# Performance work log

Measured on AMD Instinct MI355X. Metric: run time of the kernel, lower is better.

The kernel has to match this reference:

```python
import jax, jax.numpy as jnp
import numpy as np

EMBED = 1024

def setup_inputs() -> dict:
    key = jax.random.key(0)
    kx, kq, kk, kv = jax.random.split(key, 4)
    x = jax.random.normal(kx, (4, 2048, EMBED), dtype=jnp.float32)
    s = 1.0 / np.sqrt(EMBED)
    Wq = jax.random.normal(kq, (EMBED, EMBED), dtype=jnp.float32) * s
    Wk = jax.random.normal(kk, (EMBED, EMBED), dtype=jnp.float32) * s
    Wv = jax.random.normal(kv, (EMBED, EMBED), dtype=jnp.float32) * s
    return {"x": x, "Wq": Wq, "Wk": Wk, "Wv": Wv}

def reference(x, Wq, Wk, Wv):
    # x: [b, s, e]; nn.Linear(y) = y @ W.T, weights stored [out, in]
    Q = jnp.einsum('bse,oe->bso', x, Wq)
    K = jnp.einsum('bse,oe->bso', x, Wk)
    V = jnp.einsum('bse,oe->bso', x, Wv)
    scale = 1.0 / jnp.sqrt(jnp.asarray(x.shape[-1], x.dtype))
    energy = jnp.einsum('bqe,bke->bqk', Q, K) * scale  # [b, s, s]
    attention = jax.nn.softmax(energy, axis=-1)
    out = jnp.einsum('bqk,bke->bqe', attention, V)
    return out
```

## Files before the change

### kernel.cpp

```cpp
#include <hip/hip_runtime.h>
#include <stdint.h>


typedef __attribute__((ext_vector_type(8))) short bf16x8;
typedef __attribute__((ext_vector_type(4))) float f32x4;

__device__ __forceinline__ float bf2f(uint16_t u) {
    return __uint_as_float(((uint32_t)u) << 16);
}
__device__ __forceinline__ uint16_t f2bf(float f) {
    uint32_t u = __float_as_uint(f);
    uint32_t r = u + 0x7FFFu + ((u >> 16) & 1u);
    return (uint16_t)(r >> 16);
}

__device__ __forceinline__ void gll16(const void* g, void* l) {
    __builtin_amdgcn_global_load_lds(
        (const __attribute__((address_space(1))) uint32_t*)g,
        (__attribute__((address_space(3))) uint32_t*)l,
        16, 0, 0);
}

__global__ __launch_bounds__(256) void cast_all(const float* __restrict__ x,
                                                const float* __restrict__ Wq,
                                                const float* __restrict__ Wk,
                                                const float* __restrict__ Wv,
                                                uint16_t* __restrict__ xb,
                                                uint16_t* __restrict__ wqkvb,
                                                int NX4, int NW4) {
    int i = blockIdx.x * 256 + threadIdx.x;
    const float* src;
    uint16_t* dst;
    int off;
    if (i < NX4) {
        src = x; dst = xb; off = i;
    } else {
        int j = i - NX4;
        if (j >= 3 * NW4) return;
        int which = j / NW4;
        off = j - which * NW4;
        src = (which == 0) ? Wq : (which == 1) ? Wk : Wv;
        dst = wqkvb + (size_t)which * NW4 * 4;
    }
    float4 v = ((const float4*)src)[off];
    ushort4 o;
    o.x = f2bf(v.x); o.y = f2bf(v.y); o.z = f2bf(v.z); o.w = f2bf(v.w);
    ((ushort4*)dst)[off] = o;
}

__global__ __launch_bounds__(256) void softmax_rows(uint16_t* __restrict__ P) {
    const int n = 2048;
    uint16_t* row = P + (size_t)blockIdx.x * n;
    int tid = threadIdx.x;
    int w = tid >> 6, ln = tid & 63;
    float v[8];
    float m = -3.4e38f;
    #pragma unroll
    for (int i = 0; i < 8; i++) { v[i] = bf2f(row[tid + 256 * i]); m = fmaxf(m, v[i]); }
    #pragma unroll
    for (int o = 32; o >= 1; o >>= 1) m = fmaxf(m, __shfl_down(m, o, 64));
    __shared__ float smax[4], ssum[4];
    if (ln == 0) smax[w] = m;
    __syncthreads();
    m = fmaxf(fmaxf(smax[0], smax[1]), fmaxf(smax[2], smax[3]));
    float s = 0.f;
    #pragma unroll
    for (int i = 0; i < 8; i++) { v[i] = __expf(v[i] - m); s += v[i]; }
    #pragma unroll
    for (int o = 32; o >= 1; o >>= 1) s += __shfl_down(s, o, 64);
    if (ln == 0) ssum[w] = s;
    __syncthreads();
    s = ssum[0] + ssum[1] + ssum[2] + ssum[3];
    float inv = 1.f / s;
    #pragma unroll
    for (int i = 0; i < 8; i++) row[tid + 256 * i] = f2bf(v[i] * inv);
}

#define BM 128
#define BN 128
#define BK 32

template <typename OutT>
__global__ __launch_bounds__(256) void gemm_nt(const uint16_t* __restrict__ A,
                                               const uint16_t* __restrict__ B,
                                               OutT* __restrict__ C,
                                               int gx, int gy,
                                               long lda, long ldb, long ldc,
                                               int K, float alpha,
                                               long sA, long sB, long sC,
                                               uint16_t* __restrict__ VtP,
                                               int vcol0) {
    const int total = gridDim.x;
    const int n     = blockIdx.x;
    const int per   = total >> 3;
    const int g     = (n & 7) * per + (n >> 3);
    const int pb    = gx * gy;
    const int bz    = g / pb;
    const int r     = g - bz * pb;
    const int stpr  = gx >> 3;
    const int st    = r >> 6;
    const int w     = r & 63;
    const int sty   = st / stpr;
    const int stx   = st - sty * stpr;
    const int bx    = (stx << 3) + (w & 7);
    const int by    = (sty << 3) + (w >> 3);

    A += (long)bz * sA;
    B += (long)bz * sB;
    C += (long)bz * sC;

    __shared__ uint16_t As[3][BM * BK];
    __shared__ uint16_t Bs[3][BM * BK];

    const int tid  = threadIdx.x;
    const int m0   = by * BM;
    const int n0   = bx * BN;
    const int wave = tid >> 6;
    const int lane = tid & 63;
    const int quad = lane >> 4;
    const int l16  = lane & 15;
    const int wr   = (wave >> 1) * 64;
    const int wc   = (wave & 1) * 64;

    const int sr = tid >> 2;
    const int sc = (tid & 3) * 8;
    const uint16_t* Ag = A + (long)(m0 + sr) * lda + sc;
    const uint16_t* Bg = B + (long)(n0 + sr) * ldb + sc;
    const long rsA = 64 * lda;
    const long rsB = 64 * ldb;
    const int so0 = sr * BK + sc;
    const int so1 = (sr + 64) * BK + sc;

    const int nk = K / BK;

    gll16(Ag,       &As[0][so0]);
    gll16(Ag + rsA, &As[0][so1]);
    gll16(Bg,       &Bs[0][so0]);
    gll16(Bg + rsB, &Bs[0][so1]);
    Ag += BK; Bg += BK;
    gll16(Ag,       &As[1][so0]);
    gll16(Ag + rsA, &As[1][so1]);
    gll16(Bg,       &Bs[1][so0]);
    gll16(Bg + rsB, &Bs[1][so1]);
    Ag += BK; Bg += BK;

    f32x4 acc[4][4] = {};
    int cur = 0, pf = 2;

    for (int k = 0; k < nk; ++k) {
        if (k < nk - 1) {
            asm volatile("s_waitcnt vmcnt(4)\n\ts_barrier" ::: "memory");
        } else {
            asm volatile("s_waitcnt vmcnt(0)\n\ts_barrier" ::: "memory");
        }

        if (k + 2 < nk) {
            gll16(Ag,       &As[pf][so0]);
            gll16(Ag + rsA, &As[pf][so1]);
            gll16(Bg,       &Bs[pf][so0]);
            gll16(Bg + rsB, &Bs[pf][so1]);
            Ag += BK; Bg += BK;
        }

        const uint16_t* Ac = As[cur];
        const uint16_t* Bc = Bs[cur];
        const int ko = quad * 8;
        bf16x8 af[4], bfr[4];
        #pragma unroll
        for (int i = 0; i < 4; i++)
            af[i] = *(const bf16x8*)(&Ac[(wr + i * 16 + l16) * BK + ko]);
        #pragma unroll
        for (int j = 0; j < 4; j++)
            bfr[j] = *(const bf16x8*)(&Bc[(wc + j * 16 + l16) * BK + ko]);
        #pragma unroll
        for (int i = 0; i < 4; i++)
            #pragma unroll
            for (int j = 0; j < 4; j++)
                acc[i][j] = __builtin_amdgcn_mfma_f32_16x16x32_bf16(af[i], bfr[j], acc[i][j], 0, 0, 0);

        cur = (cur == 2) ? 0 : cur + 1;
        pf  = (pf  == 2) ? 0 : pf + 1;
    }

    if (VtP && n0 >= vcol0) {
        #pragma unroll
        for (int i = 0; i < 4; i++) {
            const int row0 = m0 + wr + i * 16 + quad * 4;
            const int b    = row0 >> 11;
            const int s    = row0 & 2047;
            #pragma unroll
            for (int j = 0; j < 4; j++) {
                const int e = n0 + wc + j * 16 + l16 - vcol0;
                ushort4 o;
                o.x = f2bf(acc[i][j][0]);
                o.y = f2bf(acc[i][j][1]);
                o.z = f2bf(acc[i][j][2]);
                o.w = f2bf(acc[i][j][3]);
                *(ushort4*)(VtP + ((long)b * 1024 + e) * 2048 + s) = o;
            }
        }
    } else {
        #pragma unroll
        for (int i = 0; i < 4; i++) {
            #pragma unroll
            for (int j = 0; j < 4; j++) {
                #pragma unroll
                for (int r4 = 0; r4 < 4; r4++) {
                    int row = m0 + wr + i * 16 + quad * 4 + r4;
                    int col = n0 + wc + j * 16 + l16;
                    float val = acc[i][j][r4] * alpha;
                    if constexpr (sizeof(OutT) == 2)
                        C[(long)row * ldc + col] = f2bf(val);
                    else
                        C[(long)row * ldc + col] = val;
                }
            }
        }
    }
}

extern "C" void kernel_launch(void* const* d_in, const int* in_sizes, int n_in,
                              void* d_out, int out_size, void* d_ws, size_t ws_size,
                              hipStream_t stream) {
    const float* x  = (const float*)d_in[0];
    const float* Wq = (const float*)d_in[1];
    const float* Wk = (const float*)d_in[2];
    const float* Wv = (const float*)d_in[3];
    float* out = (float*)d_out;

    const int Bn = 4, S = 2048, E = 1024;
    const long MS = (long)Bn * S;
    const int  N3 = 3 * E;

    char* ws = (char*)d_ws;
    uint16_t* xb    = (uint16_t*)ws;  ws += (size_t)MS * E * 2;
    uint16_t* wqkvb = (uint16_t*)ws;  ws += (size_t)N3 * E * 2;
    uint16_t* QKb   = (uint16_t*)ws;  ws += (size_t)MS * 2048 * 2;
    uint16_t* Vt    = (uint16_t*)ws;  ws += (size_t)Bn * E * S * 2;
    uint16_t* Pb    = (uint16_t*)ws;  ws += (size_t)Bn * S * S * 2;

    dim3 blk(256);

    {
        int NX4 = (int)(MS * E / 4);
        int NW4 = E * E / 4;
        int tot = NX4 + 3 * NW4;
        cast_all<<<dim3((tot + 255) / 256), blk, 0, stream>>>(
            x, Wq, Wk, Wv, xb, wqkvb, NX4, NW4);
    }

    {
        int gx = N3 / BN, gy = (int)(MS / BM);
        gemm_nt<uint16_t><<<dim3(gx * gy), blk, 0, stream>>>(
            xb, wqkvb, QKb, gx, gy, E, E, 2048, E, 1.f, 0, 0, 0,
            Vt, 2048);
    }

    {
        int gx = S / BN, gy = S / BM;
        gemm_nt<uint16_t><<<dim3(gx * gy * Bn), blk, 0, stream>>>(
            QKb, QKb + 1024, Pb, gx, gy, 2048, 2048, S, E, 0.03125f,
            (long)S * 2048, (long)S * 2048, (long)S * S,
            nullptr, 0);
    }

    softmax_rows<<<dim3(Bn * S), blk, 0, stream>>>(Pb);

    {
        int gx = E / BN, gy = S / BM;
        gemm_nt<float><<<dim3(gx * gy * Bn), blk, 0, stream>>>(
            Pb, Vt, out, gx, gy, S, S, E, S, 1.f,
            (long)S * S, (long)E * S, (long)S * E,
            nullptr, 0);
    }
}
```

Before: 273.7 us.

## Rewrite GEMM with 256-wide tiles, 8 waves, swizzled LDS and phased MFMA scheduling

The bf16 NT GEMM moves from 128x128x32 tiles with 4 waves and a triple buffer to 256x256 (or 128x256) tiles with BK=64, 8 waves, and a double buffer. LDS rows are XOR-swizzled to avoid bank conflicts. Loads and MFMAs are interleaved in four phases, using s_setprio and barriers to overlap global prefetch with compute. The larger tiles cut global traffic per FLOP, but they raise register and LDS pressure and lower block count, so the grid may be too small to fill the CUs.

```diff
diff --git a/kernel.cpp b/kernel.cpp
--- a/kernel.cpp
+++ b/kernel.cpp
@@ -19,6 +19,14 @@
         (const __attribute__((address_space(1))) uint32_t*)g,
         (__attribute__((address_space(3))) uint32_t*)l,
         16, 0, 0);
+}
+
+template <int NC>
+__device__ __forceinline__ void stageT(const uint16_t* g, long stride,
+                                       uint16_t* l, int tid) {
+    #pragma unroll
+    for (int c = 0; c < NC; ++c)
+        gll16(g + (long)c * 64 * stride, l + c * 4096 + tid * 8);
 }
 
 __global__ __launch_bounds__(256) void cast_all(const float* __restrict__ x,
@@ -76,139 +84,152 @@
     for (int i = 0; i < 8; i++) row[tid + 256 * i] = f2bf(v[i] * inv);
 }
 
-#define BM 128
-#define BN 128
-#define BK 32
-
-template <typename OutT>
-__global__ __launch_bounds__(256) void gemm_nt(const uint16_t* __restrict__ A,
-                                               const uint16_t* __restrict__ B,
-                                               OutT* __restrict__ C,
-                                               int gx, int gy,
-                                               long lda, long ldb, long ldc,
-                                               int K, float alpha,
-                                               long sA, long sB, long sC,
-                                               uint16_t* __restrict__ VtP,
-                                               int vcol0) {
+
+#define DS_A(mh_) do { \
+    _Pragma("unroll") for (int f_ = 0; f_ < MH; ++f_) { \
+        const uint16_t* p_ = Asb + axbase + ((mh_)*MH + f_) * 1024; \
+        af[f_][0] = *(const bf16x8*)(p_ + cs0); \
+        af[f_][1] = *(const bf16x8*)(p_ + cs1); \
+    } } while (0)
+
+#define DS_B(nh_) do { \
+    _Pragma("unroll") for (int n_ = 0; n_ < 2; ++n_) { \
+        const uint16_t* p_ = Bsb + bxbase + ((nh_)*2 + n_) * 1024; \
+        bf[nh_][n_][0] = *(const bf16x8*)(p_ + cs0); \
+        bf[nh_][n_][1] = *(const bf16x8*)(p_ + cs1); \
+    } } while (0)
+
+#define MMA(mh_, nh_) do { \
+    _Pragma("unroll") for (int f_ = 0; f_ < MH; ++f_) { \
+        _Pragma("unroll") for (int n_ = 0; n_ < 2; ++n_) { \
+            acc[(mh_)*MH + f_][(nh_)*2 + n_] = __builtin_amdgcn_mfma_f32_16x16x32_bf16( \
+                af[f_][0], bf[nh_][n_][0], acc[(mh_)*MH + f_][(nh_)*2 + n_], 0, 0, 0); \
+            acc[(mh_)*MH + f_][(nh_)*2 + n_] = __builtin_amdgcn_mfma_f32_16x16x32_bf16( \
+                af[f_][1], bf[nh_][n_][1], acc[(mh_)*MH + f_][(nh_)*2 + n_], 0, 0, 0); \
+        } } } while (0)
+
+#define PH_ENTER do { \
+    asm volatile("s_barrier\n\ts_waitcnt lgkmcnt(0)" ::: "memory"); \
+    __builtin_amdgcn_s_setprio(1); } while (0)
+
+#define PH_EXIT do { \
+    __builtin_amdgcn_s_setprio(0); \
+    asm volatile("s_barrier" ::: "memory"); } while (0)
+
+template <int BM, typename OutT>
+__global__ __launch_bounds__(512, 2) void gemm_nt(const uint16_t* __restrict__ A,
+                                                  const uint16_t* __restrict__ B,
+                                                  OutT* __restrict__ C,
+                                                  int gx, int gy,
+                                                  long lda, long ldb, long ldc,
+                                                  int K, float alpha,
+                                                  long sA, long sB, long sC,
+                                                  uint16_t* __restrict__ VtP,
+                                                  int vcol0) {
+    constexpr int MF  = BM / 32;
+    constexpr int MH  = MF / 2;
+    constexpr int NAC = BM / 64;
+
     const int total = gridDim.x;
-    const int n     = blockIdx.x;
-    const int per   = total >> 3;
-    const int g     = (n & 7) * per + (n >> 3);
-    const int pb    = gx * gy;
-    const int bz    = g / pb;
-    const int r     = g - bz * pb;
-    const int stpr  = gx >> 3;
-    const int st    = r >> 6;
-    const int w     = r & 63;
-    const int sty   = st / stpr;
-    const int stx   = st - sty * stpr;
-    const int bx    = (stx << 3) + (w & 7);
-    const int by    = (sty << 3) + (w >> 3);
+    const int nb  = blockIdx.x;
+    const int per = total >> 3;
+    const int g   = (nb & 7) * per + (nb >> 3);
+    const int pb  = gx * gy;
+    const int bz  = g / pb;
+    const int r   = g - bz * pb;
+    const int stpr = gx >> 2;
+    const int st  = r >> 4;
+    const int w   = r & 15;
+    const int sty = st / stpr;
+    const int stx = st - sty * stpr;
+    const int bx  = (stx << 2) + (w & 3);
+    const int by  = (sty << 2) + (w >> 2);
 
     A += (long)bz * sA;
     B += (long)bz * sB;
     C += (long)bz * sC;
 
-    __shared__ uint16_t As[3][BM * BK];
-    __shared__ uint16_t Bs[3][BM * BK];
-
-    const int tid  = threadIdx.x;
-    const int m0   = by * BM;
-    const int n0   = bx * BN;
-    const int wave = tid >> 6;
-    const int lane = tid & 63;
-    const int quad = lane >> 4;
-    const int l16  = lane & 15;
-    const int wr   = (wave >> 1) * 64;
-    const int wc   = (wave & 1) * 64;
-
-    const int sr = tid >> 2;
-    const int sc = (tid & 3) * 8;
-    const uint16_t* Ag = A + (long)(m0 + sr) * lda + sc;
-    const uint16_t* Bg = B + (long)(n0 + sr) * ldb + sc;
-    const long rsA = 64 * lda;
-    const long rsB = 64 * ldb;
-    const int so0 = sr * BK + sc;
-    const int so1 = (sr + 64) * BK + sc;
-
-    const int nk = K / BK;
-
-    gll16(Ag,       &As[0][so0]);
-    gll16(Ag + rsA, &As[0][so1]);
-    gll16(Bg,       &Bs[0][so0]);
-    gll16(Bg + rsB, &Bs[0][so1]);
-    Ag += BK; Bg += BK;
-    gll16(Ag,       &As[1][so0]);
-    gll16(Ag + rsA, &As[1][so1]);
-    gll16(Bg,       &Bs[1][so0]);
-    gll16(Bg + rsB, &Bs[1][so1]);
-    Ag += BK; Bg += BK;
-
-    f32x4 acc[4][4] = {};
-    int cur = 0, pf = 2;
-
-    for (int k = 0; k < nk; ++k) {
-        if (k < nk - 1) {
-            asm volatile("s_waitcnt vmcnt(4)\n\ts_barrier" ::: "memory");
-        } else {
-            asm volatile("s_waitcnt vmcnt(0)\n\ts_barrier" ::: "memory");
-        }
-
-        if (k + 2 < nk) {
-            gll16(Ag,       &As[pf][so0]);
-            gll16(Ag + rsA, &As[pf][so1]);
-            gll16(Bg,       &Bs[pf][so0]);
-            gll16(Bg + rsB, &Bs[pf][so1]);
-            Ag += BK; Bg += BK;
-        }
-
-        const uint16_t* Ac = As[cur];
-        const uint16_t* Bc = Bs[cur];
-        const int ko = quad * 8;
-        bf16x8 af[4], bfr[4];
-        #pragma unroll
-        for (int i = 0; i < 4; i++)
-            af[i] = *(const bf16x8*)(&Ac[(wr + i * 16 + l16) * BK + ko]);
-        #pragma unroll
-        for (int j = 0; j < 4; j++)
-            bfr[j] = *(const bf16x8*)(&Bc[(wc + j * 16 + l16) * BK + ko]);
-        #pragma unroll
-        for (int i = 0; i < 4; i++)
-            #pragma unroll
-            for (int j = 0; j < 4; j++)
-                acc[i][j] = __builtin_amdgcn_mfma_f32_16x16x32_bf16(af[i], bfr[j], acc[i][j], 0, 0, 0);
-
-        cur = (cur == 2) ? 0 : cur + 1;
-        pf  = (pf  == 2) ? 0 : pf + 1;
+    __shared__ uint16_t As[2][BM * 64];
+    __shared__ uint16_t Bs[2][256 * 64];
+
+    const int tid = threadIdx.x;
+    const int m0 = by * BM;
+    const int n0 = bx * 256;
+
+    const int srow = tid >> 3;
+    const int sx   = ((tid & 7) ^ (srow & 7)) << 3;
+    const uint16_t* Ag = A + (long)(m0 + srow) * lda + sx;
+    const uint16_t* Bg = B + (long)(n0 + srow) * ldb + sx;
+
+    const int wave = tid >> 6, lane = tid & 63;
+    const int quad = lane >> 4, l16 = lane & 15;
+    const int wm = wave >> 2, wn = wave & 3;
+    const int cs0 = ((quad       ^ (l16 & 7)) << 3);
+    const int cs1 = (((quad + 4) ^ (l16 & 7)) << 3);
+    const int axbase = (wm * (BM / 2) + l16) * 64;
+    const int bxbase = (wn * 64 + l16) * 64;
+
+    const int nk = K / 64;
+
+    f32x4 acc[MF][4] = {};
+    bf16x8 af[MH][2];
+    bf16x8 bf[2][2][2];
+
+    stageT<NAC>(Ag, lda, &As[0][0], tid);
+    stageT<4>(Bg, ldb, &Bs[0][0], tid);
+    asm volatile("s_waitcnt vmcnt(0)" ::: "memory");
+    asm volatile("s_barrier" ::: "memory");
+
+    for (int kt = 0; kt < nk; ++kt) {
+        const int cur = kt & 1, nxt = cur ^ 1;
+        const uint16_t* Asb = &As[cur][0];
+        const uint16_t* Bsb = &Bs[cur][0];
+        const bool pf = (kt + 1 < nk);
+        const long ko = (long)(kt + 1) * 64;
+
+        DS_A(0); DS_B(0);
+        if (pf) stageT<NAC>(Ag + ko, lda, &As[nxt][0], tid);
+        PH_ENTER; MMA(0, 0); PH_EXIT;
+
+        DS_B(1);
+        if (pf) stageT<4>(Bg + ko, ldb, &Bs[nxt][0], tid);
+        PH_ENTER; MMA(0, 1); PH_EXIT;
+
+        DS_A(1);
+        PH_ENTER; MMA(1, 0); PH_EXIT;
+
+        PH_ENTER; MMA(1, 1);
+        __builtin_amdgcn_s_setprio(0);
+        asm volatile("s_waitcnt vmcnt(0)\n\ts_barrier" ::: "memory");
     }
 
     if (VtP && n0 >= vcol0) {
         #pragma unroll
-        for (int i = 0; i < 4; i++) {
-            const int row0 = m0 + wr + i * 16 + quad * 4;
-            const int b    = row0 >> 11;
-            const int s    = row0 & 2047;
+        for (int f = 0; f < MF; ++f) {
+            const int row0 = m0 + wm * (BM / 2) + f * 16 + quad * 4;
+            const int b_   = row0 >> 11;
+            const int s_   = row0 & 2047;
             #pragma unroll
-            for (int j = 0; j < 4; j++) {
-                const int e = n0 + wc + j * 16 + l16 - vcol0;
+            for (int j = 0; j < 4; ++j) {
+                const int e = n0 + wn * 64 + j * 16 + l16 - vcol0;
                 ushort4 o;
-                o.x = f2bf(acc[i][j][0]);
-                o.y = f2bf(acc[i][j][1]);
-                o.z = f2bf(acc[i][j][2]);
-                o.w = f2bf(acc[i][j][3]);
-                *(ushort4*)(VtP + ((long)b * 1024 + e) * 2048 + s) = o;
+                o.x = f2bf(acc[f][j][0]);
+                o.y = f2bf(acc[f][j][1]);
+                o.z = f2bf(acc[f][j][2]);
+                o.w = f2bf(acc[f][j][3]);
+                *(ushort4*)(VtP + ((long)b_ * 1024 + e) * 2048 + s_) = o;
             }
         }
     } else {
         #pragma unroll
-        for (int i = 0; i < 4; i++) {
+        for (int f = 0; f < MF; ++f) {
             #pragma unroll
-            for (int j = 0; j < 4; j++) {
+            for (int j = 0; j < 4; ++j) {
                 #pragma unroll
-                for (int r4 = 0; r4 < 4; r4++) {
-                    int row = m0 + wr + i * 16 + quad * 4 + r4;
-                    int col = n0 + wc + j * 16 + l16;
-                    float val = acc[i][j][r4] * alpha;
+                for (int r4 = 0; r4 < 4; ++r4) {
+                    const int row = m0 + wm * (BM / 2) + f * 16 + quad * 4 + r4;
+                    const int col = n0 + wn * 64 + j * 16 + l16;
+                    const float val = acc[f][j][r4] * alpha;
                     if constexpr (sizeof(OutT) == 2)
                         C[(long)row * ldc + col] = f2bf(val);
                     else
@@ -239,36 +260,34 @@
     uint16_t* Vt    = (uint16_t*)ws;  ws += (size_t)Bn * E * S * 2;
     uint16_t* Pb    = (uint16_t*)ws;  ws += (size_t)Bn * S * S * 2;
 
-    dim3 blk(256);
-
     {
         int NX4 = (int)(MS * E / 4);
         int NW4 = E * E / 4;
         int tot = NX4 + 3 * NW4;
-        cast_all<<<dim3((tot + 255) / 256), blk, 0, stream>>>(
+        cast_all<<<dim3((tot + 255) / 256), dim3(256), 0, stream>>>(
             x, Wq, Wk, Wv, xb, wqkvb, NX4, NW4);
     }
 
     {
-        int gx = N3 / BN, gy = (int)(MS / BM);
-        gemm_nt<uint16_t><<<dim3(gx * gy), blk, 0, stream>>>(
+        int gx = N3 / 256, gy = (int)(MS / 256);
+        gemm_nt<256, uint16_t><<<dim3(gx * gy), dim3(512), 0, stream>>>(
             xb, wqkvb, QKb, gx, gy, E, E, 2048, E, 1.f, 0, 0, 0,
             Vt, 2048);
     }
 
     {
-        int gx = S / BN, gy = S / BM;
-        gemm_nt<uint16_t><<<dim3(gx * gy * Bn), blk, 0, stream>>>(
+        int gx = S / 256, gy = S / 256;
+        gemm_nt<256, uint16_t><<<dim3(gx * gy * Bn), dim3(512), 0, stream>>>(
             QKb, QKb + 1024, Pb, gx, gy, 2048, 2048, S, E, 0.03125f,
             (long)S * 2048, (long)S * 2048, (long)S * S,
             nullptr, 0);
     }
 
-    softmax_rows<<<dim3(Bn * S), blk, 0, stream>>>(Pb);
-
-    {
-        int gx = E / BN, gy = S / BM;
-        gemm_nt<float><<<dim3(gx * gy * Bn), blk, 0, stream>>>(
+    softmax_rows<<<dim3(Bn * S), dim3(256), 0, stream>>>(Pb);
+
+    {
+        int gx = E / 256, gy = S / 128;
+        gemm_nt<128, float><<<dim3(gx * gy * Bn), dim3(512), 0, stream>>>(
             Pb, Vt, out, gx, gy, S, S, E, S, 1.f,
             (long)S * S, (long)E * S, (long)S * E,
             nullptr, 0);
```

Measured after the change: 255.6 us. 1.07x faster.

## Swizzle GEMM LDS tile layout and vectorize softmax row access

Applied to the files above, without the earlier changes.

Gives the GEMM's shared-memory tiles an XOR-swizzled layout. Each thread's global-to-LDS load goes to a linear LDS slot while its source row and column are permuted, and the MFMA fragment reads use a matching swizzled lane offset. This is meant to cut LDS bank conflicts on the 16-byte fragment reads. Separately, the softmax kernel now loads and stores each thread's 8 bf16 values as one contiguous 16-byte vector instead of 8 strided scalar accesses. The softmax order of elements per thread changes but the reductions are order-insensitive.

```diff
diff --git a/kernel.cpp b/kernel.cpp
--- a/kernel.cpp
+++ b/kernel.cpp
@@ -49,14 +49,14 @@
 }
 
 __global__ __launch_bounds__(256) void softmax_rows(uint16_t* __restrict__ P) {
-    const int n = 2048;
-    uint16_t* row = P + (size_t)blockIdx.x * n;
-    int tid = threadIdx.x;
-    int w = tid >> 6, ln = tid & 63;
+    uint16_t* row = P + (size_t)blockIdx.x * 2048;
+    const int tid = threadIdx.x;
+    const int w = tid >> 6, ln = tid & 63;
+    bf16x8 xv = *(const bf16x8*)(&row[tid * 8]);
     float v[8];
     float m = -3.4e38f;
     #pragma unroll
-    for (int i = 0; i < 8; i++) { v[i] = bf2f(row[tid + 256 * i]); m = fmaxf(m, v[i]); }
+    for (int i = 0; i < 8; i++) { v[i] = bf2f((uint16_t)xv[i]); m = fmaxf(m, v[i]); }
     #pragma unroll
     for (int o = 32; o >= 1; o >>= 1) m = fmaxf(m, __shfl_down(m, o, 64));
     __shared__ float smax[4], ssum[4];
@@ -72,8 +72,10 @@
     __syncthreads();
     s = ssum[0] + ssum[1] + ssum[2] + ssum[3];
     float inv = 1.f / s;
-    #pragma unroll
-    for (int i = 0; i < 8; i++) row[tid + 256 * i] = f2bf(v[i] * inv);
+    bf16x8 ov;
+    #pragma unroll
+    for (int i = 0; i < 8; i++) ov[i] = (short)f2bf(v[i] * inv);
+    *(bf16x8*)(&row[tid * 8]) = ov;
 }
 
 #define BM 128
@@ -122,14 +124,15 @@
     const int wr   = (wave >> 1) * 64;
     const int wc   = (wave & 1) * 64;
 
-    const int sr = tid >> 2;
-    const int sc = (tid & 3) * 8;
-    const uint16_t* Ag = A + (long)(m0 + sr) * lda + sc;
-    const uint16_t* Bg = B + (long)(n0 + sr) * ldb + sc;
+    const int e_st = (tid & 7) ^ ((tid >> 3) & 7);
+    const int srow = ((tid >> 3) << 1) | (e_st >> 2);
+    const int scol = (e_st & 3) << 3;
+    const uint16_t* Ag = A + (long)(m0 + srow) * lda + scol;
+    const uint16_t* Bg = B + (long)(n0 + srow) * ldb + scol;
     const long rsA = 64 * lda;
     const long rsB = 64 * ldb;
-    const int so0 = sr * BK + sc;
-    const int so1 = (sr + 64) * BK + sc;
+    const int so0 = tid * 8;
+    const int so1 = tid * 8 + 2048;
 
     const int nk = K / BK;
 
@@ -144,6 +147,9 @@
     gll16(Bg + rsB, &Bs[1][so1]);
     Ag += BK; Bg += BK;
 
+    const int h = l16 >> 1;
+    const int laneOff = h * 64 + (((quad + ((l16 & 1) << 2)) ^ h) << 3);
+
     f32x4 acc[4][4] = {};
     int cur = 0, pf = 2;
 
@@ -164,14 +170,13 @@
 
         const uint16_t* Ac = As[cur];
         const uint16_t* Bc = Bs[cur];
-        const int ko = quad * 8;
         bf16x8 af[4], bfr[4];
         #pragma unroll
         for (int i = 0; i < 4; i++)
-            af[i] = *(const bf16x8*)(&Ac[(wr + i * 16 + l16) * BK + ko]);
+            af[i] = *(const bf16x8*)(&Ac[wr * 32 + i * 512 + laneOff]);
         #pragma unroll
         for (int j = 0; j < 4; j++)
-            bfr[j] = *(const bf16x8*)(&Bc[(wc + j * 16 + l16) * BK + ko]);
+            bfr[j] = *(const bf16x8*)(&Bc[wc * 32 + j * 512 + laneOff]);
         #pragma unroll
         for (int i = 0; i < 4; i++)
             #pragma unroll
```

Measured after the change: 260.3 us (median of 2 runs). -4.9%, faster.
